# Kernel optimization log

Measured on AMD Instinct MI355X. Metric: run time of the kernel, lower is better.

## Reference

```python
import jax, jax.numpy as jnp
import numpy as np

B, S, H, NH = 8, 2048, 128, 4
HS = H // NH
EPS = 1e-8


def setup_inputs() -> dict:
    key = jax.random.key(0)
    ks = jax.random.split(key, 20)
    sc = 1.0 / np.sqrt(H)
    d = {
        'item_embeds': jax.random.normal(ks[0], (B, S, H), jnp.float32),
        'behavior_embeds': jax.random.normal(ks[1], (B, S, H), jnp.float32),
        'attn_mask': jnp.zeros((B, 1, S, S), jnp.float32),
    }
    names = ['Wq', 'Wk', 'Wv', 'Wqb', 'Wkb', 'Wvb', 'Wf']
    for i, n in enumerate(names):
        d[n] = jax.random.normal(ks[2 + i], (H, H), jnp.float32) * sc
        d['b' + n[1:]] = jnp.zeros((H,), jnp.float32)
    d['ln_w'] = jnp.ones((H,), jnp.float32)
    d['ln_b'] = jnp.zeros((H,), jnp.float32)
    return d


def _split_heads(x):
    # [B,S,H] -> [B,NH,S,HS]
    return x.reshape(B, S, NH, HS).transpose(0, 2, 1, 3)


def _layer_norm(x, w, b):
    u = jnp.mean(x, -1, keepdims=True)
    s = jnp.mean((x - u) ** 2, -1, keepdims=True)
    return w * ((x - u) / jnp.sqrt(s + EPS)) + b


def reference(item_embeds, behavior_embeds, attn_mask,
              Wq, bq, Wk, bk, Wv, bv,
              Wqb, bqb, Wkb, bkb, Wvb, bvb,
              Wf, bf, ln_w, ln_b):
    Q = _split_heads(item_embeds @ Wq + bq)
    K = _split_heads(item_embeds @ Wk + bk)
    V = _split_heads(item_embeds @ Wv + bv)
    Qb = _split_heads(behavior_embeds @ Wqb + bqb)
    Kb = _split_heads(behavior_embeds @ Wkb + bkb)
    # V_behavior computed in the original forward but unused downstream
    _Vb = _split_heads(behavior_embeds @ Wvb + bvb)
    scores = (jnp.einsum('bhqd,bhkd->bhqk', Q, K)
              + jnp.einsum('bhqd,bhkd->bhqk', Qb, Kb)) / np.sqrt(HS)
    scores = scores + attn_mask
    probs = jax.nn.softmax(scores, axis=-1)
    attn_out = jnp.einsum('bhqk,bhkd->bhqd', probs, V)
    attn_out = attn_out.transpose(0, 2, 1, 3).reshape(B, S, H)
    out = attn_out @ Wf + bf
    return _layer_norm(out + item_embeds, ln_w, ln_b)
```

## Files before the change

kernel.cpp:

```cpp
#include <hip/hip_runtime.h>
#include <math.h>

typedef unsigned short ushort_t;
typedef __attribute__((ext_vector_type(8))) short bf16x8;
typedef __attribute__((ext_vector_type(4))) float f32x4;

namespace {
constexpr int B = 8, S = 2048, H = 128, NH = 4, HS = 32;
constexpr float EPS = 1e-8f;
constexpr float SCALE = 0.17677669529663687f;
constexpr int QT = 16, KT = 64;
constexpr int NE = B * S * H;
}

__device__ __forceinline__ ushort_t f2bf(float f) {
  unsigned u = __float_as_uint(f);
  unsigned r = (u + 0x7FFFu + ((u >> 16) & 1u)) >> 16;
  return (ushort_t)r;
}

__device__ __forceinline__ f32x4 mfma16(bf16x8 a, bf16x8 b, f32x4 c) {
  return __builtin_amdgcn_mfma_f32_16x16x32_bf16(a, b, c, 0, 0, 0);
}

__global__ __launch_bounds__(256) void mflag_kernel(
    const float* __restrict__ mask, unsigned* __restrict__ fm)
{
  const int qt = blockIdx.x;
  const int b  = blockIdx.y;
  const int t = threadIdx.x;
  __shared__ unsigned fmask;
  if (t == 0) fmask = 0u;
  __syncthreads();
  const float* mp = mask + ((long)b * S + (long)qt * QT) * S + t * 8;
  float s = 0.f;
#pragma unroll 4
  for (int row = 0; row < QT; ++row) {
    const float4 a = *(const float4*)&mp[(long)row * S];
    const float4 c = *(const float4*)&mp[(long)row * S + 4];
    s += fabsf(a.x) + fabsf(a.y) + fabsf(a.z) + fabsf(a.w)
       + fabsf(c.x) + fabsf(c.y) + fabsf(c.z) + fabsf(c.w);
  }
  s += __shfl_xor(s, 1);
  s += __shfl_xor(s, 2);
  s += __shfl_xor(s, 4);
  if ((t & 7) == 0 && !(s == 0.f)) atomicOr(&fmask, 1u << (t >> 3));
  __syncthreads();
  if (t == 0) fm[b * (S / QT) + qt] = fmask;
}

__global__ __launch_bounds__(256) void wcvt_kernel(
    const float* __restrict__ Wq, const float* __restrict__ Wk, const float* __restrict__ Wv,
    const float* __restrict__ Wqb, const float* __restrict__ Wkb, const float* __restrict__ Wf,
    ushort_t* __restrict__ Wt)
{
  const float* Ws[6] = {Wq, Wk, Wv, Wqb, Wkb, Wf};
  const float scl[6] = {SCALE, 1.f, 1.f, SCALE, 1.f, 1.f};
  const int m = blockIdx.y;
  const int kb = blockIdx.x;
  const float* W = Ws[m];
  const float sc = scl[m];
  __shared__ float T[32 * 132];
  const int t = threadIdx.x;
#pragma unroll
  for (int u = 0; u < 4; ++u) {
    const int idx = u * 256 + t;
    const int row = idx >> 5, c4 = idx & 31;
    const float4 v = *(const float4*)&W[(kb * 32 + row) * H + c4 * 4];
    *(float4*)&T[row * 132 + c4 * 4] = v;
  }
  __syncthreads();
#pragma unroll
  for (int u = 0; u < 16; ++u) {
    const int idx = u * 256 + t;
    const int n = idx >> 5, kk = idx & 31;
    Wt[m * (H * H) + n * H + kb * 32 + kk] = f2bf(T[kk * 132 + n] * sc);
  }
}

__global__ __launch_bounds__(256) void proj_kernel(
    const float* __restrict__ item, const float* __restrict__ beh,
    const ushort_t* __restrict__ Wt,
    const float* __restrict__ bq, const float* __restrict__ bk, const float* __restrict__ bv,
    const float* __restrict__ bqb, const float* __restrict__ bkb,
    ushort_t* __restrict__ Qo, ushort_t* __restrict__ Ko, ushort_t* __restrict__ Qbo,
    ushort_t* __restrict__ Kbo, ushort_t* __restrict__ Vto)
{
  __shared__ ushort_t Xi[16 * 136];
  __shared__ ushort_t Xb[16 * 136];
  __shared__ ushort_t Yb[5][16 * 136];
  const int t = threadIdx.x;
  const long r0 = (long)blockIdx.x * 16;
#pragma unroll
  for (int u = 0; u < 2; ++u) {
    const int idx = u * 256 + t;
    const int row = idx >> 5, c4 = idx & 31;
    const float4 vi = *(const float4*)&item[(r0 + row) * H + c4 * 4];
    const float4 vb = *(const float4*)&beh[(r0 + row) * H + c4 * 4];
    unsigned long long pi = (unsigned long long)f2bf(vi.x) | ((unsigned long long)f2bf(vi.y) << 16)
        | ((unsigned long long)f2bf(vi.z) << 32) | ((unsigned long long)f2bf(vi.w) << 48);
    unsigned long long pb = (unsigned long long)f2bf(vb.x) | ((unsigned long long)f2bf(vb.y) << 16)
        | ((unsigned long long)f2bf(vb.z) << 32) | ((unsigned long long)f2bf(vb.w) << 48);
    *(unsigned long long*)&Xi[row * 136 + c4 * 4] = pi;
    *(unsigned long long*)&Xb[row * 136 + c4 * 4] = pb;
  }
  __syncthreads();

  const int w = t >> 6, l = t & 63, l15 = l & 15, quad = l >> 4;
  const int bb = (int)(r0 >> 11);
  const int s0 = (int)(r0 & (S - 1));
  const float* bias[5] = {bq, bk, bv, bqb, bkb};
  const float bscale[5] = {SCALE, 1.f, 1.f, SCALE, 1.f};

  bf16x8 afi[4], afb[4];
#pragma unroll
  for (int ks = 0; ks < 4; ++ks) {
    afi[ks] = *(const bf16x8*)&Xi[l15 * 136 + ks * 32 + quad * 8];
    afb[ks] = *(const bf16x8*)&Xb[l15 * 136 + ks * 32 + quad * 8];
  }

#pragma unroll
  for (int p = 0; p < 5; ++p) {
    f32x4 acc[2];
#pragma unroll
    for (int nt = 0; nt < 2; ++nt) {
      const float bcol = bias[p][w * 32 + nt * 16 + l15] * bscale[p];
      acc[nt] = (f32x4){bcol, bcol, bcol, bcol};
    }
    const ushort_t* Wp = Wt + p * (H * H);
    const bf16x8* af = (p < 3) ? afi : afb;
#pragma unroll
    for (int ks = 0; ks < 4; ++ks) {
      bf16x8 bfr[2];
#pragma unroll
      for (int nt = 0; nt < 2; ++nt)
        bfr[nt] = *(const bf16x8*)&Wp[(w * 32 + nt * 16 + l15) * H + ks * 32 + quad * 8];
#pragma unroll
      for (int nt = 0; nt < 2; ++nt)
        acc[nt] = mfma16(af[ks], bfr[nt], acc[nt]);
    }
#pragma unroll
    for (int nt = 0; nt < 2; ++nt)
#pragma unroll
      for (int r = 0; r < 4; ++r)
        Yb[p][(quad * 4 + r) * 136 + w * 32 + nt * 16 + l15] = f2bf(acc[nt][r]);
  }
  __syncthreads();
  {
    const int row = t >> 4, cb = (t & 15) * 8;
    const int h = cb >> 5, dd = cb & 31;
    const long gidx = ((long)(bb * NH + h) * S + s0 + row) * HS + dd;
    ushort_t* dsts4[4] = {Qo, Ko, Qbo, Kbo};
    const int psrc[4] = {0, 1, 3, 4};
#pragma unroll
    for (int i = 0; i < 4; ++i)
      *(uint4*)&dsts4[i][gidx] = *(const uint4*)&Yb[psrc[i]][row * 136 + cb];
    const int d = t >> 1, sh = (t & 1) * 8;
    ushort_t tmp[8];
#pragma unroll
    for (int i = 0; i < 8; ++i) tmp[i] = Yb[2][(sh + i) * 136 + d];
    const long vidx = ((long)(bb * NH + (d >> 5)) * HS + (d & 31)) * S + s0 + sh;
    *(uint4*)&Vto[vidx] = *(const uint4*)&tmp[0];
  }
}

__device__ __forceinline__ void attn_step(
    int k0, int kn, bool msknz,
    const bf16x8 (&kfc)[4], const bf16x8 (&kbfc)[4],
    bf16x8 (&kfn)[4], bf16x8 (&kbfn)[4],
    const bf16x8& qf, const bf16x8& qbf,
    const ushort_t* __restrict__ K, const ushort_t* __restrict__ Kb,
    const ushort_t* __restrict__ Vt,
    long hQ, long hV, const float* const (&mrow)[4],
    int l15, int quad, ushort_t* Pw,
    float (&lsum)[4], f32x4 (&O)[2])
{
  bf16x8 vf[2][2];
#pragma unroll
  for (int dt = 0; dt < 2; ++dt)
#pragma unroll
    for (int ks = 0; ks < 2; ++ks)
      vf[dt][ks] = *(const bf16x8*)&Vt[hV + (long)(dt * 16 + l15) * S + k0 + ks * 32 + quad * 8];
#pragma unroll
  for (int nt = 0; nt < 4; ++nt) {
    kfn[nt]  = *(const bf16x8*)&K[hQ + (long)(kn + nt * 16 + l15) * HS + quad * 8];
    kbfn[nt] = *(const bf16x8*)&Kb[hQ + (long)(kn + nt * 16 + l15) * HS + quad * 8];
  }
  f32x4 sc[4];
  if (msknz) {
#pragma unroll
    for (int nt = 0; nt < 4; ++nt)
#pragma unroll
      for (int r = 0; r < 4; ++r)
        sc[nt][r] = mrow[r][k0 + nt * 16];
  } else {
#pragma unroll
    for (int nt = 0; nt < 4; ++nt)
      sc[nt] = (f32x4){0.f, 0.f, 0.f, 0.f};
  }
#pragma unroll
  for (int nt = 0; nt < 4; ++nt) {
    sc[nt] = mfma16(qbf, kbfc[nt], sc[nt]);
    sc[nt] = mfma16(qf, kfc[nt], sc[nt]);
  }
#pragma unroll
  for (int nt = 0; nt < 4; ++nt)
#pragma unroll
    for (int r = 0; r < 4; ++r)
      sc[nt][r] = __expf(sc[nt][r]);
#pragma unroll
  for (int r = 0; r < 4; ++r)
    lsum[r] += sc[0][r] + sc[1][r] + sc[2][r] + sc[3][r];
#pragma unroll
  for (int nt = 0; nt < 4; ++nt)
#pragma unroll
    for (int r = 0; r < 4; ++r)
      Pw[(quad * 4 + r) * 72 + nt * 16 + l15] = f2bf(sc[nt][r]);
  bf16x8 pf[2];
#pragma unroll
  for (int ks = 0; ks < 2; ++ks)
    pf[ks] = *(const bf16x8*)&Pw[l15 * 72 + ks * 32 + quad * 8];
#pragma unroll
  for (int dt = 0; dt < 2; ++dt)
#pragma unroll
    for (int ks = 0; ks < 2; ++ks)
      O[dt] = mfma16(pf[ks], vf[dt][ks], O[dt]);
}

__global__ __launch_bounds__(256, 3) void attn_kernel(
    const ushort_t* __restrict__ Q, const ushort_t* __restrict__ K,
    const ushort_t* __restrict__ Qb, const ushort_t* __restrict__ Kb,
    const ushort_t* __restrict__ Vt, const float* __restrict__ mask,
    const unsigned* __restrict__ fmg, ushort_t* __restrict__ attn_out)
{
  __shared__ ushort_t Pb[NH][16 * 72];
  const int t = threadIdx.x;
  const int w = t >> 6;
  const int l15 = t & 15, quad = (t & 63) >> 4;
  const int q0 = blockIdx.x * QT;
  const int b = blockIdx.y;
  const long hQ = (long)(b * NH + w) * S * HS;
  const long hV = (long)(b * NH + w) * HS * S;

  const bf16x8 qf  = *(const bf16x8*)&Q[hQ + (long)(q0 + l15) * HS + quad * 8];
  const bf16x8 qbf = *(const bf16x8*)&Qb[hQ + (long)(q0 + l15) * HS + quad * 8];

  const unsigned fm = fmg[b * (S / QT) + blockIdx.x];

  const float* mrow[4];
#pragma unroll
  for (int r = 0; r < 4; ++r)
    mrow[r] = mask + ((long)b * S + q0 + quad * 4 + r) * S + l15;

  float lsum[4] = {0.f, 0.f, 0.f, 0.f};
  f32x4 O[2];
#pragma unroll
  for (int dt = 0; dt < 2; ++dt) O[dt] = (f32x4){0.f, 0.f, 0.f, 0.f};
  ushort_t* Pw = Pb[w];

  bf16x8 kfA[4], kbfA[4], kfB[4], kbfB[4];
#pragma unroll
  for (int nt = 0; nt < 4; ++nt) {
    kfA[nt]  = *(const bf16x8*)&K[hQ + (long)(nt * 16 + l15) * HS + quad * 8];
    kbfA[nt] = *(const bf16x8*)&Kb[hQ + (long)(nt * 16 + l15) * HS + quad * 8];
  }

  for (int kt = 0; kt < S / KT; kt += 2) {
    const int k0 = kt * KT;
    const int kn1 = k0 + KT;
    const int kn2 = (kt + 2 < S / KT) ? k0 + 2 * KT : k0;
    attn_step(k0, kn1, (fm >> kt) & 1u, kfA, kbfA, kfB, kbfB,
              qf, qbf, K, Kb, Vt, hQ, hV, mrow, l15, quad, Pw, lsum, O);
    attn_step(kn1, kn2, (fm >> (kt + 1)) & 1u, kfB, kbfB, kfA, kbfA,
              qf, qbf, K, Kb, Vt, hQ, hV, mrow, l15, quad, Pw, lsum, O);
  }
#pragma unroll
  for (int r = 0; r < 4; ++r) {
    float s = lsum[r];
    s += __shfl_xor(s, 1);
    s += __shfl_xor(s, 2);
    s += __shfl_xor(s, 4);
    s += __shfl_xor(s, 8);
    lsum[r] = s;
  }
#pragma unroll
  for (int r = 0; r < 4; ++r) {
    const float inv = 1.f / lsum[r];
    const long row = (long)b * S + q0 + quad * 4 + r;
#pragma unroll
    for (int dt = 0; dt < 2; ++dt)
      attn_out[row * H + w * 32 + dt * 16 + l15] = f2bf(O[dt][r] * inv);
  }
}

__global__ __launch_bounds__(256) void out_kernel(
    const ushort_t* __restrict__ attn, const float* __restrict__ item,
    const ushort_t* __restrict__ Wft, const float* __restrict__ bf_,
    const float* __restrict__ lnw, const float* __restrict__ lnb,
    float* __restrict__ out)
{
  __shared__ ushort_t As[16 * 136];
  __shared__ float Ys[16 * 132];
  const int t = threadIdx.x;
  const long r0 = (long)blockIdx.x * 16;
  {
    const int row = t >> 4, c8 = t & 15;
    *(uint4*)&As[row * 136 + c8 * 8] = *(const uint4*)&attn[(r0 + row) * H + c8 * 8];
  }
  __syncthreads();
  const int w = t >> 6, l15 = t & 15, quad = (t & 63) >> 4;
  f32x4 acc[2];
#pragma unroll
  for (int nt = 0; nt < 2; ++nt) {
    const float bcol = bf_[w * 32 + nt * 16 + l15];
    acc[nt] = (f32x4){bcol, bcol, bcol, bcol};
  }
#pragma unroll
  for (int ks = 0; ks < 4; ++ks) {
    const bf16x8 a = *(const bf16x8*)&As[l15 * 136 + ks * 32 + quad * 8];
#pragma unroll
    for (int nt = 0; nt < 2; ++nt) {
      const bf16x8 bfr = *(const bf16x8*)&Wft[(w * 32 + nt * 16 + l15) * H + ks * 32 + quad * 8];
      acc[nt] = mfma16(a, bfr, acc[nt]);
    }
  }
#pragma unroll
  for (int nt = 0; nt < 2; ++nt)
#pragma unroll
    for (int r = 0; r < 4; ++r) {
      const int rl = quad * 4 + r;
      const int col = w * 32 + nt * 16 + l15;
      Ys[rl * 132 + col] = acc[nt][r] + item[(r0 + rl) * H + col];
    }
  __syncthreads();
  const int rl = t >> 4, ch = t & 15;
  float v[8];
#pragma unroll
  for (int g = 0; g < 2; ++g) {
    const float4 y = *(const float4*)&Ys[rl * 132 + ch * 8 + g * 4];
    v[g * 4 + 0] = y.x; v[g * 4 + 1] = y.y; v[g * 4 + 2] = y.z; v[g * 4 + 3] = y.w;
  }
  float s = 0.f;
#pragma unroll
  for (int i = 0; i < 8; ++i) s += v[i];
  s += __shfl_xor(s, 1);
  s += __shfl_xor(s, 2);
  s += __shfl_xor(s, 4);
  s += __shfl_xor(s, 8);
  const float u_ = s * (1.f / H);
  float s2 = 0.f;
#pragma unroll
  for (int i = 0; i < 8; ++i) { const float d = v[i] - u_; s2 += d * d; }
  s2 += __shfl_xor(s2, 1);
  s2 += __shfl_xor(s2, 2);
  s2 += __shfl_xor(s2, 4);
  s2 += __shfl_xor(s2, 8);
  const float rinv = rsqrtf(s2 * (1.f / H) + EPS);
#pragma unroll
  for (int g = 0; g < 2; ++g) {
    float4 o;
    const int col = ch * 8 + g * 4;
    o.x = lnw[col + 0] * ((v[g * 4 + 0] - u_) * rinv) + lnb[col + 0];
    o.y = lnw[col + 1] * ((v[g * 4 + 1] - u_) * rinv) + lnb[col + 1];
    o.z = lnw[col + 2] * ((v[g * 4 + 2] - u_) * rinv) + lnb[col + 2];
    o.w = lnw[col + 3] * ((v[g * 4 + 3] - u_) * rinv) + lnb[col + 3];
    *(float4*)&out[(r0 + rl) * H + col] = o;
  }
}

extern "C" void kernel_launch(void* const* d_in, const int* in_sizes, int n_in,
                              void* d_out, int out_size, void* d_ws, size_t ws_size,
                              hipStream_t stream) {
  const float* item = (const float*)d_in[0];
  const float* beh  = (const float*)d_in[1];
  const float* mask = (const float*)d_in[2];
  const float* Wq  = (const float*)d_in[3];  const float* bq  = (const float*)d_in[4];
  const float* Wk  = (const float*)d_in[5];  const float* bk  = (const float*)d_in[6];
  const float* Wv  = (const float*)d_in[7];  const float* bv  = (const float*)d_in[8];
  const float* Wqb = (const float*)d_in[9];  const float* bqb = (const float*)d_in[10];
  const float* Wkb = (const float*)d_in[11]; const float* bkb = (const float*)d_in[12];
  const float* Wf  = (const float*)d_in[15]; const float* bfv = (const float*)d_in[16];
  const float* lnw = (const float*)d_in[17]; const float* lnb = (const float*)d_in[18];
  float* out = (float*)d_out;

  ushort_t* ws = (ushort_t*)d_ws;
  ushort_t* Qw   = ws;
  ushort_t* Kw   = Qw + NE;
  ushort_t* Qbw  = Kw + NE;
  ushort_t* Kbw  = Qbw + NE;
  ushort_t* Vtw  = Kbw + NE;
  ushort_t* Attw = Vtw + NE;
  ushort_t* Wt   = Attw + NE;
  unsigned* fm   = (unsigned*)(Wt + 6 * H * H);

  mflag_kernel<<<dim3(S / QT, B), 256, 0, stream>>>(mask, fm);
  wcvt_kernel<<<dim3(4, 6), 256, 0, stream>>>(Wq, Wk, Wv, Wqb, Wkb, Wf, Wt);
  proj_kernel<<<dim3((B * S) / 16), 256, 0, stream>>>(
      item, beh, Wt, bq, bk, bv, bqb, bkb, Qw, Kw, Qbw, Kbw, Vtw);
  attn_kernel<<<dim3(S / QT, B), 256, 0, stream>>>(
      Qw, Kw, Qbw, Kbw, Vtw, mask, fm, Attw);
  out_kernel<<<dim3((B * S) / 16), 256, 0, stream>>>(
      Attw, item, Wt + 5 * H * H, bfv, lnw, lnb, out);
}
```

Before: 390.4 us.

## Split attention over keys in two halves and combine partials in a new kernel

Splits the key dimension of the attention kernel into two halves along a new grid z axis. Each half writes unnormalized bf16 partial outputs and row sums, and a new combine kernel adds them and normalizes. It also folds log2(e) into the Q scale so the kernel can use exp2, truncates P to bf16 instead of rounding, raises the occupancy hint, and widens the mask-flag kernel's grid using global atomics after a memset. This adds parallelism and occupancy, at the cost of an extra kernel launch and extra partial-output traffic, with slight precision loss from bf16 partials and truncation.

Result: slower. 808.6 us (+107.1%).

```diff
diff --git a/kernel.cpp b/kernel.cpp
--- a/kernel.cpp
+++ b/kernel.cpp
@@ -9,7 +9,11 @@
 constexpr int B = 8, S = 2048, H = 128, NH = 4, HS = 32;
 constexpr float EPS = 1e-8f;
 constexpr float SCALE = 0.17677669529663687f;
+constexpr float LOG2E = 1.4426950408889634f;
+constexpr float SCALEL = SCALE * LOG2E;
 constexpr int QT = 16, KT = 64;
+constexpr int KS = 2;
+constexpr int SKT = S / KS / KT;
 constexpr int NE = B * S * H;
 }
 
@@ -28,25 +32,26 @@
 {
   const int qt = blockIdx.x;
   const int b  = blockIdx.y;
+  const int z  = blockIdx.z;
   const int t = threadIdx.x;
-  __shared__ unsigned fmask;
-  if (t == 0) fmask = 0u;
-  __syncthreads();
-  const float* mp = mask + ((long)b * S + (long)qt * QT) * S + t * 8;
+  const int lt = t >> 6;
+  const int lane = t & 63;
+  const float* mp = mask + ((long)b * S + (long)qt * QT + (lane >> 4) * 4) * S
+                  + z * 256 + lt * 64 + (lane & 15) * 4;
   float s = 0.f;
-#pragma unroll 4
-  for (int row = 0; row < QT; ++row) {
-    const float4 a = *(const float4*)&mp[(long)row * S];
-    const float4 c = *(const float4*)&mp[(long)row * S + 4];
-    s += fabsf(a.x) + fabsf(a.y) + fabsf(a.z) + fabsf(a.w)
-       + fabsf(c.x) + fabsf(c.y) + fabsf(c.z) + fabsf(c.w);
+#pragma unroll
+  for (int rr = 0; rr < 4; ++rr) {
+    const float4 a = *(const float4*)&mp[(long)rr * S];
+    s += fabsf(a.x) + fabsf(a.y) + fabsf(a.z) + fabsf(a.w);
   }
   s += __shfl_xor(s, 1);
   s += __shfl_xor(s, 2);
   s += __shfl_xor(s, 4);
-  if ((t & 7) == 0 && !(s == 0.f)) atomicOr(&fmask, 1u << (t >> 3));
-  __syncthreads();
-  if (t == 0) fm[b * (S / QT) + qt] = fmask;
+  s += __shfl_xor(s, 8);
+  s += __shfl_xor(s, 16);
+  s += __shfl_xor(s, 32);
+  if (lane == 0 && !(s == 0.f))
+    atomicOr(&fm[b * (S / QT) + qt], 1u << (z * 4 + lt));
 }
 
 __global__ __launch_bounds__(256) void wcvt_kernel(
@@ -55,7 +60,7 @@
     ushort_t* __restrict__ Wt)
 {
   const float* Ws[6] = {Wq, Wk, Wv, Wqb, Wkb, Wf};
-  const float scl[6] = {SCALE, 1.f, 1.f, SCALE, 1.f, 1.f};
+  const float scl[6] = {SCALEL, 1.f, 1.f, SCALEL, 1.f, 1.f};
   const int m = blockIdx.y;
   const int kb = blockIdx.x;
   const float* W = Ws[m];
@@ -110,7 +115,7 @@
   const int bb = (int)(r0 >> 11);
   const int s0 = (int)(r0 & (S - 1));
   const float* bias[5] = {bq, bk, bv, bqb, bkb};
-  const float bscale[5] = {SCALE, 1.f, 1.f, SCALE, 1.f};
+  const float bscale[5] = {SCALEL, 1.f, 1.f, SCALEL, 1.f};
 
   bf16x8 afi[4], afb[4];
 #pragma unroll
@@ -192,7 +197,7 @@
     for (int nt = 0; nt < 4; ++nt)
 #pragma unroll
       for (int r = 0; r < 4; ++r)
-        sc[nt][r] = mrow[r][k0 + nt * 16];
+        sc[nt][r] = mrow[r][k0 + nt * 16] * LOG2E;
   } else {
 #pragma unroll
     for (int nt = 0; nt < 4; ++nt)
@@ -207,7 +212,7 @@
   for (int nt = 0; nt < 4; ++nt)
 #pragma unroll
     for (int r = 0; r < 4; ++r)
-      sc[nt][r] = __expf(sc[nt][r]);
+      sc[nt][r] = __builtin_amdgcn_exp2f(sc[nt][r]);
 #pragma unroll
   for (int r = 0; r < 4; ++r)
     lsum[r] += sc[0][r] + sc[1][r] + sc[2][r] + sc[3][r];
@@ -215,7 +220,8 @@
   for (int nt = 0; nt < 4; ++nt)
 #pragma unroll
     for (int r = 0; r < 4; ++r)
-      Pw[(quad * 4 + r) * 72 + nt * 16 + l15] = f2bf(sc[nt][r]);
+      Pw[(quad * 4 + r) * 72 + nt * 16 + l15] =
+          (ushort_t)(__float_as_uint(sc[nt][r]) >> 16);
   bf16x8 pf[2];
 #pragma unroll
   for (int ks = 0; ks < 2; ++ks)
@@ -227,11 +233,12 @@
       O[dt] = mfma16(pf[ks], vf[dt][ks], O[dt]);
 }
 
-__global__ __launch_bounds__(256, 3) void attn_kernel(
+__global__ __launch_bounds__(256, 8) void attn_kernel(
     const ushort_t* __restrict__ Q, const ushort_t* __restrict__ K,
     const ushort_t* __restrict__ Qb, const ushort_t* __restrict__ Kb,
     const ushort_t* __restrict__ Vt, const float* __restrict__ mask,
-    const unsigned* __restrict__ fmg, ushort_t* __restrict__ attn_out)
+    const unsigned* __restrict__ fmg,
+    ushort_t* __restrict__ PO, float* __restrict__ lsumP)
 {
   __shared__ ushort_t Pb[NH][16 * 72];
   const int t = threadIdx.x;
@@ -239,6 +246,8 @@
   const int l15 = t & 15, quad = (t & 63) >> 4;
   const int q0 = blockIdx.x * QT;
   const int b = blockIdx.y;
+  const int kz = blockIdx.z;
+  const int kbase = kz * (S / KS);
   const long hQ = (long)(b * NH + w) * S * HS;
   const long hV = (long)(b * NH + w) * HS * S;
 
@@ -261,17 +270,17 @@
   bf16x8 kfA[4], kbfA[4], kfB[4], kbfB[4];
 #pragma unroll
   for (int nt = 0; nt < 4; ++nt) {
-    kfA[nt]  = *(const bf16x8*)&K[hQ + (long)(nt * 16 + l15) * HS + quad * 8];
-    kbfA[nt] = *(const bf16x8*)&Kb[hQ + (long)(nt * 16 + l15) * HS + quad * 8];
-  }
-
-  for (int kt = 0; kt < S / KT; kt += 2) {
-    const int k0 = kt * KT;
+    kfA[nt]  = *(const bf16x8*)&K[hQ + (long)(kbase + nt * 16 + l15) * HS + quad * 8];
+    kbfA[nt] = *(const bf16x8*)&Kb[hQ + (long)(kbase + nt * 16 + l15) * HS + quad * 8];
+  }
+
+  for (int i = 0; i < SKT; i += 2) {
+    const int k0 = kbase + i * KT;
     const int kn1 = k0 + KT;
-    const int kn2 = (kt + 2 < S / KT) ? k0 + 2 * KT : k0;
-    attn_step(k0, kn1, (fm >> kt) & 1u, kfA, kbfA, kfB, kbfB,
+    const int kn2 = (i + 2 < SKT) ? k0 + 2 * KT : kbase;
+    attn_step(k0, kn1, (fm >> (kz * SKT + i)) & 1u, kfA, kbfA, kfB, kbfB,
               qf, qbf, K, Kb, Vt, hQ, hV, mrow, l15, quad, Pw, lsum, O);
-    attn_step(kn1, kn2, (fm >> (kt + 1)) & 1u, kfB, kbfB, kfA, kbfA,
+    attn_step(kn1, kn2, (fm >> (kz * SKT + i + 1)) & 1u, kfB, kbfB, kfA, kbfA,
               qf, qbf, K, Kb, Vt, hQ, hV, mrow, l15, quad, Pw, lsum, O);
   }
 #pragma unroll
@@ -285,12 +294,43 @@
   }
 #pragma unroll
   for (int r = 0; r < 4; ++r) {
-    const float inv = 1.f / lsum[r];
     const long row = (long)b * S + q0 + quad * 4 + r;
 #pragma unroll
     for (int dt = 0; dt < 2; ++dt)
-      attn_out[row * H + w * 32 + dt * 16 + l15] = f2bf(O[dt][r] * inv);
-  }
+      PO[(long)kz * NE + row * H + w * 32 + dt * 16 + l15] = f2bf(O[dt][r]);
+    if (l15 == 0)
+      lsumP[((long)(kz * B + b) * NH + w) * S + q0 + quad * 4 + r] = lsum[r];
+  }
+}
+
+__global__ __launch_bounds__(256) void comb_kernel(
+    const ushort_t* __restrict__ PO, const float* __restrict__ lsumP,
+    ushort_t* __restrict__ attn_out)
+{
+  const long idx8 = ((long)blockIdx.x * 256 + threadIdx.x) * 8;
+  const int col = (int)(idx8 & (H - 1));
+  const long row = idx8 >> 7;
+  const int b = (int)(row >> 11);
+  const int s = (int)(row & (S - 1));
+  const int h = col >> 5;
+  const float l = lsumP[((long)(0 * B + b) * NH + h) * S + s]
+                + lsumP[((long)(1 * B + b) * NH + h) * S + s];
+  const float inv = 1.f / l;
+  const uint4 a0 = *(const uint4*)&PO[idx8];
+  const uint4 a1 = *(const uint4*)&PO[(long)NE + idx8];
+  uint4 res;
+  const unsigned av0[4] = {a0.x, a0.y, a0.z, a0.w};
+  const unsigned av1[4] = {a1.x, a1.y, a1.z, a1.w};
+  unsigned rv[4];
+#pragma unroll
+  for (int i = 0; i < 4; ++i) {
+    const float lo = (__uint_as_float(av0[i] << 16) + __uint_as_float(av1[i] << 16)) * inv;
+    const float hi = (__uint_as_float(av0[i] & 0xFFFF0000u)
+                    + __uint_as_float(av1[i] & 0xFFFF0000u)) * inv;
+    rv[i] = (unsigned)f2bf(lo) | ((unsigned)f2bf(hi) << 16);
+  }
+  res.x = rv[0]; res.y = rv[1]; res.z = rv[2]; res.w = rv[3];
+  *(uint4*)&attn_out[idx8] = res;
 }
 
 __global__ __launch_bounds__(256) void out_kernel(
@@ -390,15 +430,19 @@
   ushort_t* Kbw  = Qbw + NE;
   ushort_t* Vtw  = Kbw + NE;
   ushort_t* Attw = Vtw + NE;
-  ushort_t* Wt   = Attw + NE;
+  ushort_t* PO   = Attw + NE;
+  ushort_t* Wt   = PO + (long)KS * NE;
   unsigned* fm   = (unsigned*)(Wt + 6 * H * H);
-
-  mflag_kernel<<<dim3(S / QT, B), 256, 0, stream>>>(mask, fm);
+  float* lsumP   = (float*)(fm + B * (S / QT));
+
+  hipMemsetAsync(fm, 0, B * (S / QT) * sizeof(unsigned), stream);
+  mflag_kernel<<<dim3(S / QT, B, 8), 256, 0, stream>>>(mask, fm);
   wcvt_kernel<<<dim3(4, 6), 256, 0, stream>>>(Wq, Wk, Wv, Wqb, Wkb, Wf, Wt);
   proj_kernel<<<dim3((B * S) / 16), 256, 0, stream>>>(
       item, beh, Wt, bq, bk, bv, bqb, bkb, Qw, Kw, Qbw, Kbw, Vtw);
-  attn_kernel<<<dim3(S / QT, B), 256, 0, stream>>>(
-      Qw, Kw, Qbw, Kbw, Vtw, mask, fm, Attw);
+  attn_kernel<<<dim3(S / QT, B, KS), 256, 0, stream>>>(
+      Qw, Kw, Qbw, Kbw, Vtw, mask, fm, PO, lsumP);
+  comb_kernel<<<dim3(NE / (256 * 8)), 256, 0, stream>>>(PO, lsumP, Attw);
   out_kernel<<<dim3((B * S) / 16), 256, 0, stream>>>(
       Attw, item, Wt + 5 * H * H, bfv, lnw, lnb, out);
 }
```
